# Performance work log

Measured on AMD Instinct MI355X. Metric: run time of the kernel, lower is better.

The kernel has to match this reference:

```python
import jax, jax.numpy as jnp
import numpy as np

N = 50000      # nodes
E = 800000     # edges (before self-loops)
DIN = 146      # input feature dim
D = 128        # hidden/out dim
G = 64         # graphs in batch
L = 4          # number of GCNConv layers (len(hidden_dims[1:]) + 1)
NC = 10        # classes
EPS = 1e-5     # BatchNorm eps


def setup_inputs() -> dict:
    key = jax.random.key(0)
    ks = jax.random.split(key, 12)
    x = jax.random.normal(ks[0], (N, DIN), jnp.float32)
    edge_index = jax.random.randint(ks[1], (2, E), 0, N, dtype=jnp.int64)
    batch = jnp.sort(jax.random.randint(ks[2], (N,), 0, G, dtype=jnp.int64))

    def lin(k, shape, fan_in):
        return (jax.random.normal(k, shape, jnp.float32) / np.sqrt(fan_in)).astype(jnp.float32)

    W_emb = lin(ks[3], (DIN, D), DIN)
    b_emb = jnp.zeros((D,), jnp.float32)
    W_gcn = lin(ks[4], (L, D, D), D)
    b_gcn = jnp.zeros((L, D), jnp.float32)
    bn_gamma = jnp.ones((L, D), jnp.float32)
    bn_beta = jnp.zeros((L, D), jnp.float32)
    W_r1 = lin(ks[5], (D, D // 2), D)
    b_r1 = jnp.zeros((D // 2,), jnp.float32)
    W_r2 = lin(ks[6], (D // 2, D // 4), D // 2)
    b_r2 = jnp.zeros((D // 4,), jnp.float32)
    W_r3 = lin(ks[7], (D // 4, NC), D // 4)
    b_r3 = jnp.zeros((NC,), jnp.float32)
    return {"x": x, "edge_index": edge_index, "batch": batch,
            "W_emb": W_emb, "b_emb": b_emb, "W_gcn": W_gcn, "b_gcn": b_gcn,
            "bn_gamma": bn_gamma, "bn_beta": bn_beta,
            "W_r1": W_r1, "b_r1": b_r1, "W_r2": W_r2, "b_r2": b_r2,
            "W_r3": W_r3, "b_r3": b_r3}


def reference(x, edge_index, batch, W_emb, b_emb, W_gcn, b_gcn,
              bn_gamma, bn_beta, W_r1, b_r1, W_r2, b_r2, W_r3, b_r3):
    # gcn_norm with self-loops (fill_value=1, improved=False)
    loop = jnp.arange(N, dtype=edge_index.dtype)
    src = jnp.concatenate([edge_index[0], loop])
    dst = jnp.concatenate([edge_index[1], loop])
    deg = jax.ops.segment_sum(jnp.ones(src.shape, x.dtype), dst, num_segments=N)
    dinv = jax.lax.rsqrt(jnp.maximum(deg, jnp.asarray(1e-12, x.dtype)))  # deg >= 1 (self loops)
    norm = (dinv[src] * dinv[dst])[:, None]  # [E+N, 1]

    h = x @ W_emb + b_emb  # embedding_h
    for l in range(L):
        h_in = h
        m = h @ W_gcn[l]                                            # [N, D]
        h = jax.ops.segment_sum(m[src] * norm, dst, num_segments=N) + b_gcn[l]
        # BatchNorm1d (training-mode batch stats, biased var)
        mu = h.mean(axis=0)
        var = h.var(axis=0)
        h = (h - mu) * jax.lax.rsqrt(var + EPS) * bn_gamma[l] + bn_beta[l]
        h = jax.nn.relu(h)
        h = h_in + h  # residual (dims always match here)

    # global_mean_pool over batch ids
    sums = jax.ops.segment_sum(h, batch, num_segments=G)
    cnts = jax.ops.segment_sum(jnp.ones((N, 1), h.dtype), batch, num_segments=G)
    hg = sums / jnp.maximum(cnts, 1.0)

    # MLPReadout: two hidden layers halving dims, then classifier
    z = jax.nn.relu(hg @ W_r1 + b_r1)
    z = jax.nn.relu(z @ W_r2 + b_r2)
    return z @ W_r3 + b_r3  # [G, NC]
```

## Files before the change

### kernel.cpp

```cpp
#include <hip/hip_runtime.h>
#include <hip/hip_bf16.h>

#define NN 50000
#define EE 800000
#define DIN 146
#define DD 128
#define GG 64
#define LL 4
#define NC 10
#define BN_EPS 1e-5f

#define KP_EMB 160
#define AST_L  136
#define NCOPY 64
#define NPW 4
#define RST 129

#define MB_EDGE   3125
#define MB_REPACK (MB_EDGE + 31250)
#define MB_BATCH  (MB_REPACK + 196)
#define MB_PARAMS (MB_BATCH + 384)
#define MB_WT     (MB_PARAMS + 400)

typedef __attribute__((ext_vector_type(8))) short bf16x8;
typedef __attribute__((ext_vector_type(4))) float f32x4;

__device__ __forceinline__ float bf2f(__hip_bfloat16 v) { return __bfloat162float(v); }
__device__ __forceinline__ float loadf(const void* p, long i, int f32) {
    return f32 ? ((const float*)p)[i] : bf2f(((const __hip_bfloat16*)p)[i]);
}
__device__ __forceinline__ unsigned short f2bf_bits(float f) {
    __hip_bfloat16 h = __float2bfloat16(f);
    return *(unsigned short*)&h;
}
__device__ __forceinline__ float bfu2f(unsigned short u) {
    return __uint_as_float((unsigned)u << 16);
}
__device__ __forceinline__ void acc_add8(float* acc, uint4 v) {
    acc[0] += __uint_as_float(v.x << 16);
    acc[1] += __uint_as_float(v.x & 0xffff0000u);
    acc[2] += __uint_as_float(v.y << 16);
    acc[3] += __uint_as_float(v.y & 0xffff0000u);
    acc[4] += __uint_as_float(v.z << 16);
    acc[5] += __uint_as_float(v.z & 0xffff0000u);
    acc[6] += __uint_as_float(v.w << 16);
    acc[7] += __uint_as_float(v.w & 0xffff0000u);
}

__global__ void detect_kernel(const void* ei, const void* batch, const void* Wemb,
                              int* __restrict__ flags) {
    __shared__ int s_edge_nz, s_batch_nz, s_f32_cnt;
    int t = threadIdx.x;
    if (t == 0) { s_edge_nz = 0; s_batch_nz = 0; s_f32_cnt = 0; }
    __syncthreads();
    {   const int* w = (const int*)ei;
        long j = ((long)t * ((2L * EE) / 64)) | 1;
        if (w[j] != 0) atomicAdd(&s_edge_nz, 1);
    }
    {   const int* w = (const int*)batch;
        long j = ((long)(NN / 2) + (long)t * ((NN / 2) / 64)) | 1;
        if (j < NN && w[j] != 0) atomicAdd(&s_batch_nz, 1);
    }
    {   const unsigned short* w = (const unsigned short*)Wemb;
        unsigned short v = w[2 * t];
        int ex = (v >> 7) & 0xFF;
        if (v != 0 && ex >= 128) atomicAdd(&s_f32_cnt, 1);
    }
    __syncthreads();
    if (t == 0) {
        flags[0] = (s_edge_nz == 0) ? 1 : 0;
        flags[1] = (s_batch_nz == 0) ? 1 : 0;
        flags[2] = (s_f32_cnt >= 8) ? 1 : 0;
    }
}

struct Param { const void* src; float* dst; int src_n; int dst_n; };
struct Params12 { Param p[12]; };
struct WtDesc { const void* src; long src_off; unsigned short* dst; int K; int Kpad; };
struct WtDescs5 { WtDesc p[5]; };

__global__ void init_kernel(int* __restrict__ deg, float* __restrict__ statmulti,
                            float* __restrict__ hgsum) {
    int i = blockIdx.x * blockDim.x + threadIdx.x;
    if (i < NN) deg[i] = 0;
    if (i < LL * NCOPY * 256) statmulti[i] = 0.0f;
    if (i < GG * DD) hgsum[i] = 0.0f;
}

__global__ __launch_bounds__(256) void mega_pre_kernel(
    const void* __restrict__ x, const void* __restrict__ ei,
    const void* __restrict__ batch, const int* __restrict__ flags,
    unsigned short* __restrict__ xb,
    int* __restrict__ src32, int* __restrict__ dst32,
    int* __restrict__ rank, int* __restrict__ deg, int* __restrict__ b32,
    Params12 P, WtDescs5 W)
{
    int b = blockIdx.x;
    int t = threadIdx.x;
    if (b < MB_EDGE) {
        int e = b * 256 + t;
        const int* w = (const int*)ei;
        int s, d;
        if (flags[0]) { s = w[2L * e]; d = w[2L * (EE + e)]; }
        else          { s = w[e];      d = w[EE + e]; }
        src32[e] = s; dst32[e] = d;
        int r = 0;
        if ((unsigned)d < (unsigned)NN) r = atomicAdd(&deg[d], 1);
        rank[e] = r;
    } else if (b < MB_REPACK) {
        int f32 = flags[2];
        long idx = (long)(b - MB_EDGE) * 256 + t;
        int row = (int)(idx / KP_EMB);
        int k = (int)(idx - (long)row * KP_EMB);
        float v = (k < DIN) ? loadf(x, (long)row * DIN + k, f32) : 0.0f;
        xb[idx] = f2bf_bits(v);
    } else if (b < MB_BATCH) {
        int i = (b - MB_REPACK) * 256 + t;
        if (i < NN) b32[i] = flags[1] ? ((const int*)batch)[2L * i] : ((const int*)batch)[i];
    } else if (b < MB_PARAMS) {
        int f32 = flags[2];
        int bb = b - MB_BATCH;
        const Param& e = P.p[bb >> 5];
        int idx = (bb & 31) * 256 + t;
        if (idx < e.dst_n)
            e.dst[idx] = (idx < e.src_n) ? loadf(e.src, idx, f32) : 0.0f;
    } else {
        int f32 = flags[2];
        int bb = b - MB_PARAMS;
        int y = bb / 80;
        const WtDesc& e = W.p[y];
        int idx = (bb - y * 80) * 256 + t;
        if (idx < 128 * e.Kpad) {
            int n = idx / e.Kpad, k = idx - n * e.Kpad;
            float v = (k < e.K) ? loadf(e.src, e.src_off + (long)k * DD + n, f32) : 0.0f;
            e.dst[idx] = f2bf_bits(v);
        }
    }
}

__global__ void scan1_kernel(const int* __restrict__ cnt, int* __restrict__ off,
                             int* __restrict__ bsum, float* __restrict__ dinv, int n) {
    int t = threadIdx.x;
    int i = blockIdx.x * 256 + t;
    int v = (i < n) ? cnt[i] : 0;
    if (i < n) dinv[i] = rsqrtf((float)(v + 1));
    int lane = t & 63, w = t >> 6;
    int x = v;
    #pragma unroll
    for (int s = 1; s < 64; s <<= 1) {
        int y = __shfl_up(x, s, 64);
        if (lane >= s) x += y;
    }
    __shared__ int wsum[4];
    if (lane == 63) wsum[w] = x;
    __syncthreads();
    if (t == 0) {
        int a = 0;
        #pragma unroll
        for (int k = 0; k < 4; ++k) { int tmp = wsum[k]; wsum[k] = a; a += tmp; }
        bsum[blockIdx.x] = a;
    }
    __syncthreads();
    int excl = x - v + wsum[w];
    if (i < n) off[i] = excl;
}

__global__ void scan2_kernel(int* __restrict__ bsum, int* __restrict__ boff,
                             int* __restrict__ off_last, int nb) {
    int t = threadIdx.x;
    int v = (t < nb) ? bsum[t] : 0;
    int lane = t & 63, w = t >> 6;
    int x = v;
    #pragma unroll
    for (int s = 1; s < 64; s <<= 1) {
        int y = __shfl_up(x, s, 64);
        if (lane >= s) x += y;
    }
    __shared__ int wsum[4];
    if (lane == 63) wsum[w] = x;
    __syncthreads();
    __shared__ int total_s;
    if (t == 0) {
        int a = 0;
        #pragma unroll
        for (int k = 0; k < 4; ++k) { int tmp = wsum[k]; wsum[k] = a; a += tmp; }
        total_s = a;
    }
    __syncthreads();
    if (t < nb) boff[t] = x - v + wsum[w];
    if (t == 0) *off_last = total_s;
}

__global__ void scan3_kernel(int* __restrict__ off, const int* __restrict__ boff, int n) {
    int i = blockIdx.x * 256 + threadIdx.x;
    if (i < n) off[i] += boff[blockIdx.x];
}

__global__ void scatter_kernel(const int* __restrict__ src, const int* __restrict__ dst,
                               const int* __restrict__ rank, const int* __restrict__ off,
                               int* __restrict__ src_s, int E) {
    int e = blockIdx.x * blockDim.x + threadIdx.x;
    if (e >= E) return;
    int s = src[e], d = dst[e];
    if ((unsigned)s >= (unsigned)NN || (unsigned)d >= (unsigned)NN) return;
    src_s[off[d] + rank[e]] = s;
}


__global__ __launch_bounds__(256) void emb_gemm_kernel(
    const unsigned short* __restrict__ Ab,
    const unsigned short* __restrict__ Wt,
    const float* __restrict__ bias,
    float* __restrict__ h, unsigned short* __restrict__ hb, int n)
{
    int t = threadIdx.x;
    int r0 = blockIdx.x * 128;
    int lane = t & 63, w = t >> 6;
    int m = lane & 15, quad = lane >> 4;
    int rbase = r0 + w * 32;
    bf16x8 a[2][5];
    #pragma unroll
    for (int rt = 0; rt < 2; ++rt)
        #pragma unroll
        for (int c = 0; c < 5; ++c) {
            int rr = rbase + rt * 16 + m; if (rr > n - 1) rr = n - 1;
            a[rt][c] = *(const bf16x8*)(Ab + (long)rr * KP_EMB + c * 32 + quad * 8);
        }
    f32x4 acc[2][8];
    #pragma unroll
    for (int t8 = 0; t8 < 8; ++t8) {
        float bv = bias[t8 * 16 + m];
        f32x4 ai = {bv, bv, bv, bv};
        acc[0][t8] = ai; acc[1][t8] = ai;
    }
    #pragma unroll
    for (int t8 = 0; t8 < 8; ++t8) {
        #pragma unroll
        for (int c = 0; c < 5; ++c) {
            bf16x8 b = *(const bf16x8*)(Wt + (long)(t8 * 16 + m) * KP_EMB + c * 32 + quad * 8);
            acc[0][t8] = __builtin_amdgcn_mfma_f32_16x16x32_bf16(a[0][c], b, acc[0][t8], 0, 0, 0);
            acc[1][t8] = __builtin_amdgcn_mfma_f32_16x16x32_bf16(a[1][c], b, acc[1][t8], 0, 0, 0);
        }
    }
    #pragma unroll
    for (int rt = 0; rt < 2; ++rt)
        #pragma unroll
        for (int t8 = 0; t8 < 8; ++t8)
            #pragma unroll
            for (int rg = 0; rg < 4; ++rg) {
                int row = rbase + rt * 16 + quad * 4 + rg;
                int col = t8 * 16 + m;
                if (row < n) {
                    float v = acc[rt][t8][rg];
                    h[(long)row * DD + col] = v;
                    hb[(long)row * DD + col] = f2bf_bits(v);
                }
            }
}

__global__ __launch_bounds__(256) void gemm_plain_kernel(
    const unsigned short* __restrict__ Ab,
    const unsigned short* __restrict__ Wt,
    const float* __restrict__ dinv,
    unsigned short* __restrict__ Mb, int n)
{
    int t = threadIdx.x;
    int r0 = blockIdx.x * 128;
    int lane = t & 63, w = t >> 6;
    int m = lane & 15, quad = lane >> 4;
    int rbase = r0 + w * 32;
    bf16x8 a[2][4];
    #pragma unroll
    for (int rt = 0; rt < 2; ++rt)
        #pragma unroll
        for (int c = 0; c < 4; ++c) {
            int rr = rbase + rt * 16 + m; if (rr > n - 1) rr = n - 1;
            a[rt][c] = *(const bf16x8*)(Ab + (long)rr * DD + c * 32 + quad * 8);
        }
    float dv[2][4];
    #pragma unroll
    for (int rt = 0; rt < 2; ++rt)
        #pragma unroll
        for (int rg = 0; rg < 4; ++rg) {
            int row = rbase + rt * 16 + quad * 4 + rg; if (row > n - 1) row = n - 1;
            dv[rt][rg] = dinv[row];
        }
    f32x4 acc[2][8];
    #pragma unroll
    for (int t8 = 0; t8 < 8; ++t8) {
        f32x4 z = {0.f, 0.f, 0.f, 0.f};
        acc[0][t8] = z; acc[1][t8] = z;
    }
    #pragma unroll
    for (int t8 = 0; t8 < 8; ++t8) {
        #pragma unroll
        for (int c = 0; c < 4; ++c) {
            bf16x8 b = *(const bf16x8*)(Wt + (long)(t8 * 16 + m) * DD + c * 32 + quad * 8);
            acc[0][t8] = __builtin_amdgcn_mfma_f32_16x16x32_bf16(a[0][c], b, acc[0][t8], 0, 0, 0);
            acc[1][t8] = __builtin_amdgcn_mfma_f32_16x16x32_bf16(a[1][c], b, acc[1][t8], 0, 0, 0);
        }
    }
    #pragma unroll
    for (int rt = 0; rt < 2; ++rt)
        #pragma unroll
        for (int t8 = 0; t8 < 8; ++t8)
            #pragma unroll
            for (int rg = 0; rg < 4; ++rg) {
                int row = rbase + rt * 16 + quad * 4 + rg;
                int col = t8 * 16 + m;
                if (row < n) Mb[(long)row * DD + col] = f2bf_bits(dv[rt][rg] * acc[rt][t8][rg]);
            }
}

__global__ __launch_bounds__(256) void gemm_fused_kernel(
    const float* __restrict__ agg, float* __restrict__ h,
    const float* __restrict__ bnacc, const float* __restrict__ gamma,
    const float* __restrict__ beta, const float* __restrict__ dinv,
    const unsigned short* __restrict__ Wt, unsigned short* __restrict__ Mb, int n)
{
    __shared__ unsigned short As[128 * AST_L];
    int t = threadIdx.x;
    int r0 = blockIdx.x * 128;
    {
        int c4 = (t & 31) * 4, rsub = t >> 5;
        float inv_n = 1.0f / (float)n;
        float4 sm = *(const float4*)&bnacc[c4];
        float4 sq = *(const float4*)&bnacc[128 + c4];
        float4 ga = *(const float4*)&gamma[c4];
        float4 be = *(const float4*)&beta[c4];
        float4 mu, rs;
        mu.x = sm.x * inv_n; mu.y = sm.y * inv_n; mu.z = sm.z * inv_n; mu.w = sm.w * inv_n;
        rs.x = rsqrtf(sq.x * inv_n - mu.x * mu.x + BN_EPS) * ga.x;
        rs.y = rsqrtf(sq.y * inv_n - mu.y * mu.y + BN_EPS) * ga.y;
        rs.z = rsqrtf(sq.z * inv_n - mu.z * mu.z + BN_EPS) * ga.z;
        rs.w = rsqrtf(sq.w * inv_n - mu.w * mu.w + BN_EPS) * ga.w;
        #pragma unroll 4
        for (int i = 0; i < 16; ++i) {
            int row = i * 8 + rsub;
            int r = r0 + row;
            unsigned short o0 = 0, o1 = 0, o2 = 0, o3 = 0;
            if (r < n) {
                long g = (long)r * DD + c4;
                float4 av = *(const float4*)&agg[g];
                float4 hv = *(const float4*)&h[g];
                hv.x += fmaxf((av.x - mu.x) * rs.x + be.x, 0.0f);
                hv.y += fmaxf((av.y - mu.y) * rs.y + be.y, 0.0f);
                hv.z += fmaxf((av.z - mu.z) * rs.z + be.z, 0.0f);
                hv.w += fmaxf((av.w - mu.w) * rs.w + be.w, 0.0f);
                *(float4*)&h[g] = hv;
                o0 = f2bf_bits(hv.x); o1 = f2bf_bits(hv.y);
                o2 = f2bf_bits(hv.z); o3 = f2bf_bits(hv.w);
            }
            unsigned short* dst = &As[row * AST_L + c4];
            dst[0] = o0; dst[1] = o1; dst[2] = o2; dst[3] = o3;
        }
    }
    __syncthreads();
    int lane = t & 63, w = t >> 6;
    int m = lane & 15, quad = lane >> 4;
    int rl = w * 32;
    int rbase = r0 + rl;
    bf16x8 a[2][4];
    #pragma unroll
    for (int rt = 0; rt < 2; ++rt)
        #pragma unroll
        for (int c = 0; c < 4; ++c)
            a[rt][c] = *(const bf16x8*)(As + (rl + rt * 16 + m) * AST_L + c * 32 + quad * 8);
    float dv[2][4];
    #pragma unroll
    for (int rt = 0; rt < 2; ++rt)
        #pragma unroll
        for (int rg = 0; rg < 4; ++rg) {
            int row = rbase + rt * 16 + quad * 4 + rg; if (row > n - 1) row = n - 1;
            dv[rt][rg] = dinv[row];
        }
    f32x4 acc[2][8];
    #pragma unroll
    for (int t8 = 0; t8 < 8; ++t8) {
        f32x4 z = {0.f, 0.f, 0.f, 0.f};
        acc[0][t8] = z; acc[1][t8] = z;
    }
    #pragma unroll
    for (int t8 = 0; t8 < 8; ++t8) {
        #pragma unroll
        for (int c = 0; c < 4; ++c) {
            bf16x8 b = *(const bf16x8*)(Wt + (long)(t8 * 16 + m) * DD + c * 32 + quad * 8);
            acc[0][t8] = __builtin_amdgcn_mfma_f32_16x16x32_bf16(a[0][c], b, acc[0][t8], 0, 0, 0);
            acc[1][t8] = __builtin_amdgcn_mfma_f32_16x16x32_bf16(a[1][c], b, acc[1][t8], 0, 0, 0);
        }
    }
    #pragma unroll
    for (int rt = 0; rt < 2; ++rt)
        #pragma unroll
        for (int t8 = 0; t8 < 8; ++t8)
            #pragma unroll
            for (int rg = 0; rg < 4; ++rg) {
                int row = rbase + rt * 16 + quad * 4 + rg;
                int col = t8 * 16 + m;
                if (row < n) Mb[(long)row * DD + col] = f2bf_bits(dv[rt][rg] * acc[rt][t8][rg]);
            }
}

__global__ __launch_bounds__(256) void agg_kernel(
    const unsigned short* __restrict__ mb, const int* __restrict__ off,
    const int* __restrict__ src_s, const float* __restrict__ dinv,
    const float* __restrict__ bias, float* __restrict__ agg,
    float* __restrict__ statacc)
{
    __shared__ float sred[4][4 * RST];
    __shared__ float2 ssum[4][64], ssq[4][64];
    int t = threadIdx.x;
    int wv = t >> 6, lane = t & 63;
    int grp = lane >> 4, sl = lane & 15;
    float* red = sred[wv];
    float2 bi = ((const float2*)bias)[lane];
    float2 sAcc = {0.0f, 0.0f}, qAcc = {0.0f, 0.0f};
    int i0 = (blockIdx.x * 4 + wv) * NPW;
    #pragma unroll 1
    for (int ni = 0; ni < NPW; ++ni) {
        int i = i0 + ni;
        if (i >= NN) break;
        float acc[8];
        #pragma unroll
        for (int k = 0; k < 8; ++k) acc[k] = 0.0f;
        if (grp == 0) {
            uint4 v = *(const uint4*)(mb + (long)i * DD + sl * 8);
            acc_add8(acc, v);
        }
        int e = off[i], e1 = off[i + 1];
        for (; e + 8 <= e1; e += 8) {
            int ja = src_s[e + grp];
            int jb = src_s[e + 4 + grp];
            uint4 va = *(const uint4*)(mb + (long)ja * DD + sl * 8);
            uint4 vb = *(const uint4*)(mb + (long)jb * DD + sl * 8);
            acc_add8(acc, va);
            acc_add8(acc, vb);
        }
        for (; e + 4 <= e1; e += 4) {
            int j = src_s[e + grp];
            uint4 v = *(const uint4*)(mb + (long)j * DD + sl * 8);
            acc_add8(acc, v);
        }
        if (e + grp < e1) {
            int j = src_s[e + grp];
            uint4 v = *(const uint4*)(mb + (long)j * DD + sl * 8);
            acc_add8(acc, v);
        }
        #pragma unroll
        for (int k = 0; k < 8; ++k) red[grp * RST + sl * 8 + k] = acc[k];
        asm volatile("" ::: "memory");
        float c0 = 0.0f, c1 = 0.0f;
        #pragma unroll
        for (int g = 0; g < 4; ++g) {
            c0 += red[g * RST + 2 * lane];
            c1 += red[g * RST + 2 * lane + 1];
        }
        asm volatile("" ::: "memory");
        float di = dinv[i];
        float2 outv;
        outv.x = di * c0 + bi.x;
        outv.y = di * c1 + bi.y;
        ((float2*)agg)[(long)i * 64 + lane] = outv;
        sAcc.x += outv.x; sAcc.y += outv.y;
        qAcc.x += outv.x * outv.x; qAcc.y += outv.y * outv.y;
    }
    ssum[wv][lane] = sAcc; ssq[wv][lane] = qAcc;
    __syncthreads();
    if (wv == 0) {
        float2 s0 = ssum[0][lane], s1 = ssum[1][lane], s2 = ssum[2][lane], s3 = ssum[3][lane];
        float2 q0 = ssq[0][lane], q1 = ssq[1][lane], q2 = ssq[2][lane], q3 = ssq[3][lane];
        float sx = s0.x + s1.x + s2.x + s3.x;
        float sy = s0.y + s1.y + s2.y + s3.y;
        float qx = q0.x + q1.x + q2.x + q3.x;
        float qy = q0.y + q1.y + q2.y + q3.y;
        float* copy = statacc + (blockIdx.x & (NCOPY - 1)) * 256;
        atomicAdd(&copy[2 * lane], sx);
        atomicAdd(&copy[2 * lane + 1], sy);
        atomicAdd(&copy[128 + 2 * lane], qx);
        atomicAdd(&copy[128 + 2 * lane + 1], qy);
    }
}

__global__ void statfin_kernel(const float* __restrict__ multi, float* __restrict__ bnacc) {
    int c = threadIdx.x;
    float s = 0.0f;
    #pragma unroll 8
    for (int k = 0; k < NCOPY; ++k) s += multi[k * 256 + c];
    bnacc[c] = s;
}

__global__ void pool1_kernel(const float* __restrict__ h, const float* __restrict__ agg,
                             const float* __restrict__ bnacc,
                             const float* __restrict__ gamma, const float* __restrict__ beta,
                             const int* __restrict__ b32, float* __restrict__ hgsum, int n) {
    int t = threadIdx.x;
    int c4 = (t & 31) * 4, rsub = t >> 5;
    float inv_n = 1.0f / (float)n;
    float4 sm = *(const float4*)&bnacc[c4];
    float4 sq = *(const float4*)&bnacc[128 + c4];
    float4 ga = *(const float4*)&gamma[c4];
    float4 be = *(const float4*)&beta[c4];
    float4 mu, rs;
    mu.x = sm.x * inv_n; mu.y = sm.y * inv_n; mu.z = sm.z * inv_n; mu.w = sm.w * inv_n;
    rs.x = rsqrtf(sq.x * inv_n - mu.x * mu.x + BN_EPS) * ga.x;
    rs.y = rsqrtf(sq.y * inv_n - mu.y * mu.y + BN_EPS) * ga.y;
    rs.z = rsqrtf(sq.z * inv_n - mu.z * mu.z + BN_EPS) * ga.z;
    rs.w = rsqrtf(sq.w * inv_n - mu.w * mu.w + BN_EPS) * ga.w;
    int rows_pb = (n + gridDim.x - 1) / gridDim.x;
    int r0 = blockIdx.x * rows_pb;
    int r1 = min(n, r0 + rows_pb);
    float4 acc = {0, 0, 0, 0};
    int gcur = -1;
    for (int r = r0 + rsub; r < r1; r += 8) {
        int g = b32[r];
        if (g != gcur) {
            if (gcur >= 0) {
                atomicAdd(&hgsum[gcur * DD + c4 + 0], acc.x);
                atomicAdd(&hgsum[gcur * DD + c4 + 1], acc.y);
                atomicAdd(&hgsum[gcur * DD + c4 + 2], acc.z);
                atomicAdd(&hgsum[gcur * DD + c4 + 3], acc.w);
            }
            acc.x = acc.y = acc.z = acc.w = 0.0f;
            gcur = ((unsigned)g < (unsigned)GG) ? g : -1;
        }
        if (gcur >= 0) {
            long ix = (long)r * DD + c4;
            float4 av = *(const float4*)&agg[ix];
            float4 hv = *(const float4*)&h[ix];
            acc.x += hv.x + fmaxf((av.x - mu.x) * rs.x + be.x, 0.0f);
            acc.y += hv.y + fmaxf((av.y - mu.y) * rs.y + be.y, 0.0f);
            acc.z += hv.z + fmaxf((av.z - mu.z) * rs.z + be.z, 0.0f);
            acc.w += hv.w + fmaxf((av.w - mu.w) * rs.w + be.w, 0.0f);
        }
    }
    if (gcur >= 0) {
        atomicAdd(&hgsum[gcur * DD + c4 + 0], acc.x);
        atomicAdd(&hgsum[gcur * DD + c4 + 1], acc.y);
        atomicAdd(&hgsum[gcur * DD + c4 + 2], acc.z);
        atomicAdd(&hgsum[gcur * DD + c4 + 3], acc.w);
    }
}

__device__ int lower_bound_i(const int* __restrict__ a, int n, int v) {
    int lo = 0, hi = n;
    while (lo < hi) {
        int mid = (lo + hi) >> 1;
        if (a[mid] < v) lo = mid + 1; else hi = mid;
    }
    return lo;
}

__global__ void readout_kernel(const float* __restrict__ hgsum, const int* __restrict__ b32,
                               const float* __restrict__ W1, const float* __restrict__ b1,
                               const float* __restrict__ W2, const float* __restrict__ b2,
                               const float* __restrict__ W3, const float* __restrict__ b3,
                               const int* __restrict__ flags, void* __restrict__ out, int n) {
    int f32 = flags[2];
    int g = blockIdx.x;
    int t = threadIdx.x;
    __shared__ float hgs[DD];
    __shared__ float z1[DD / 2];
    __shared__ float z2[DD / 4];
    int lo = lower_bound_i(b32, n, g);
    int hi = lower_bound_i(b32, n, g + 1);
    float invc = 1.0f / fmaxf((float)(hi - lo), 1.0f);
    hgs[t] = hgsum[g * DD + t] * invc;
    __syncthreads();
    if (t < DD / 2) {
        float acc = b1[t];
        #pragma unroll 8
        for (int k = 0; k < DD; ++k) acc = fmaf(hgs[k], W1[k * (DD / 2) + t], acc);
        z1[t] = fmaxf(acc, 0.0f);
    }
    __syncthreads();
    if (t < DD / 4) {
        float acc = b2[t];
        #pragma unroll 8
        for (int k = 0; k < DD / 2; ++k) acc = fmaf(z1[k], W2[k * (DD / 4) + t], acc);
        z2[t] = fmaxf(acc, 0.0f);
    }
    __syncthreads();
    if (t < NC) {
        float acc = b3[t];
        #pragma unroll 8
        for (int k = 0; k < DD / 4; ++k) acc = fmaf(z2[k], W3[k * NC + t], acc);
        if (f32) ((float*)out)[g * NC + t] = acc;
        else     ((__hip_bfloat16*)out)[g * NC + t] = __float2bfloat16(acc);
    }
}

extern "C" void kernel_launch(void* const* d_in, const int* in_sizes, int n_in,
                              void* d_out, int out_size, void* d_ws, size_t ws_size,
                              hipStream_t stream) {
    const void* x      = d_in[0];
    const void* ei     = d_in[1];
    const void* batch  = d_in[2];
    const void* W_emb  = d_in[3];
    const void* b_emb  = d_in[4];
    const void* W_gcn  = d_in[5];
    const void* b_gcn  = d_in[6];
    const void* bn_g   = d_in[7];
    const void* bn_b   = d_in[8];
    const void* W_r1   = d_in[9];
    const void* b_r1   = d_in[10];
    const void* W_r2   = d_in[11];
    const void* b_r2   = d_in[12];
    const void* W_r3   = d_in[13];
    const void* b_r3   = d_in[14];

    char* p = (char*)d_ws;
    auto alloc = [&](size_t bytes) -> void* {
        void* r = (void*)p;
        p += (bytes + 255) & ~(size_t)255;
        return r;
    };
    int*   flags  = (int*)alloc(64 * 4);
    int*   deg    = (int*)alloc((size_t)NN * 4);
    float* bnacc  = (float*)alloc((size_t)LL * 256 * 4);
    float* statmulti = (float*)alloc((size_t)LL * NCOPY * 256 * 4);
    float* hgsum  = (float*)alloc((size_t)GG * DD * 4);
    int*   off    = (int*)alloc((size_t)(NN + 1) * 4);
    float* dinv   = (float*)alloc((size_t)NN * 4);
    int*   src32  = (int*)alloc((size_t)EE * 4);
    int*   dst32  = (int*)alloc((size_t)EE * 4);
    int*   rank   = (int*)alloc((size_t)EE * 4);
    int*   b32    = (int*)alloc((size_t)NN * 4);
    int*   src_s  = (int*)alloc((size_t)EE * 4);
    int*   bsum   = (int*)alloc(256 * 4);
    int*   boff   = (int*)alloc(256 * 4);
    float* h      = (float*)alloc((size_t)NN * DD * 4);
    unsigned short* hb = (unsigned short*)alloc((size_t)NN * DD * 2);
    unsigned short* mb = (unsigned short*)alloc((size_t)NN * DD * 2);
    float* agg    = (float*)alloc((size_t)NN * DD * 4);
    unsigned short* xb = (unsigned short*)agg;
    unsigned short* wt_emb = (unsigned short*)alloc((size_t)DD * KP_EMB * 2);
    unsigned short* wt_gcn = (unsigned short*)alloc((size_t)LL * DD * DD * 2);
    float* b_emb32 = (float*)alloc(DD * 4);
    float* b_gcn32 = (float*)alloc((size_t)LL * DD * 4);
    float* bng32   = (float*)alloc((size_t)LL * DD * 4);
    float* bnb32   = (float*)alloc((size_t)LL * DD * 4);
    float* wr1     = (float*)alloc((size_t)DD * (DD / 2) * 4);
    float* br1     = (float*)alloc((DD / 2) * 4);
    float* wr2     = (float*)alloc((size_t)(DD / 2) * (DD / 4) * 4);
    float* br2     = (float*)alloc((DD / 4) * 4);
    float* wr3     = (float*)alloc((size_t)(DD / 4) * NC * 4);
    float* br3     = (float*)alloc(NC * 4);

    detect_kernel<<<1, 64, 0, stream>>>(ei, batch, W_emb, flags);
    init_kernel<<<256, 256, 0, stream>>>(deg, statmulti, hgsum);

    Params12 P;
    P.p[0]  = { b_emb, b_emb32, DD, DD };
    P.p[1]  = { b_gcn, b_gcn32, LL * DD, LL * DD };
    P.p[2]  = { bn_g,  bng32,   LL * DD, LL * DD };
    P.p[3]  = { bn_b,  bnb32,   LL * DD, LL * DD };
    P.p[4]  = { W_r1,  wr1,     DD * (DD / 2), DD * (DD / 2) };
    P.p[5]  = { b_r1,  br1,     DD / 2, DD / 2 };
    P.p[6]  = { W_r2,  wr2,     (DD / 2) * (DD / 4), (DD / 2) * (DD / 4) };
    P.p[7]  = { b_r2,  br2,     DD / 4, DD / 4 };
    P.p[8]  = { W_r3,  wr3,     (DD / 4) * NC, (DD / 4) * NC };
    P.p[9]  = { b_r3,  br3,     NC, NC };
    P.p[10] = { b_r3,  br3,     0, 0 };
    P.p[11] = { b_r3,  br3,     0, 0 };

    WtDescs5 W;
    W.p[0] = { W_emb, 0,            wt_emb,                DIN, KP_EMB };
    W.p[1] = { W_gcn, 0L * DD * DD, wt_gcn + 0L * DD * DD, DD,  DD };
    W.p[2] = { W_gcn, 1L * DD * DD, wt_gcn + 1L * DD * DD, DD,  DD };
    W.p[3] = { W_gcn, 2L * DD * DD, wt_gcn + 2L * DD * DD, DD,  DD };
    W.p[4] = { W_gcn, 3L * DD * DD, wt_gcn + 3L * DD * DD, DD,  DD };

    mega_pre_kernel<<<MB_WT, 256, 0, stream>>>(x, ei, batch, flags, xb,
                                               src32, dst32, rank, deg, b32, P, W);

    int nb = (NN + 255) / 256;
    scan1_kernel<<<nb, 256, 0, stream>>>(deg, off, bsum, dinv, NN);
    scan2_kernel<<<1, 256, 0, stream>>>(bsum, boff, off + NN, nb);
    scan3_kernel<<<nb, 256, 0, stream>>>(off, boff, NN);

    scatter_kernel<<<(EE + 255) / 256, 256, 0, stream>>>(src32, dst32, rank, off, src_s, EE);

    int ngemm = (NN + 127) / 128;
    emb_gemm_kernel<<<ngemm, 256, 0, stream>>>(xb, wt_emb, b_emb32, h, hb, NN);

    int nagg = (NN + 4 * NPW - 1) / (4 * NPW);
    for (int l = 0; l < LL; ++l) {
        if (l == 0) {
            gemm_plain_kernel<<<ngemm, 256, 0, stream>>>(hb, wt_gcn, dinv, mb, NN);
        } else {
            gemm_fused_kernel<<<ngemm, 256, 0, stream>>>(
                agg, h, bnacc + (l - 1) * 256, bng32 + (l - 1) * DD, bnb32 + (l - 1) * DD,
                dinv, wt_gcn + (size_t)l * DD * DD, mb, NN);
        }
        agg_kernel<<<nagg, 256, 0, stream>>>(mb, off, src_s, dinv,
                                             b_gcn32 + l * DD, agg,
                                             statmulti + (size_t)l * NCOPY * 256);
        statfin_kernel<<<1, 256, 0, stream>>>(statmulti + (size_t)l * NCOPY * 256,
                                              bnacc + l * 256);
    }

    pool1_kernel<<<512, 256, 0, stream>>>(h, agg, bnacc + (LL - 1) * 256,
                                          bng32 + (LL - 1) * DD, bnb32 + (LL - 1) * DD,
                                          b32, hgsum, NN);
    readout_kernel<<<GG, DD, 0, stream>>>(hgsum, b32, wr1, br1, wr2, br2, wr3, br3,
                                          flags, d_out, NN);
}
```

Baseline: 472.3 us.

## Merge preprocessing launches and fold stat reduction into consumer kernels

Folds init_kernel into the conversion mega-kernel. The edge degree-counting blocks now share a launch with the embedding GEMM, and the CSR scatter shares a launch with the layer-0 GEMM. It also removes statfin_kernel: every gemm_fused and pool1 block now reduces the 64 stat copies itself into shared memory. The aim is to cut kernel launches and the gaps between them, and to overlap independent work. The cost is redundant stat reduction in every block plus a dependence on independent work being correctly split into separate block ranges.

New measurement: 458.4 us. 1.03x faster.

```diff
diff --git a/kernel.cpp b/kernel.cpp
--- a/kernel.cpp
+++ b/kernel.cpp
@@ -16,11 +16,16 @@
 #define NPW 4
 #define RST 129
 
-#define MB_EDGE   3125
-#define MB_REPACK (MB_EDGE + 31250)
-#define MB_BATCH  (MB_REPACK + 196)
-#define MB_PARAMS (MB_BATCH + 384)
-#define MB_WT     (MB_PARAMS + 400)
+#define C_INIT   256
+#define C_REPACK (C_INIT + 31250)
+#define C_BATCH  (C_REPACK + 196)
+#define C_PARAMS (C_BATCH + 384)
+#define C_WT     (C_PARAMS + 400)
+
+#define B_EDGE 3125
+#define B_TOT  (B_EDGE + 391)
+#define S_SCAT 3125
+#define S_TOT  (S_SCAT + 391)
 
 typedef __attribute__((ext_vector_type(8))) short bf16x8;
 typedef __attribute__((ext_vector_type(4))) float f32x4;
@@ -79,26 +84,63 @@
 struct WtDesc { const void* src; long src_off; unsigned short* dst; int K; int Kpad; };
 struct WtDescs5 { WtDesc p[5]; };
 
-__global__ void init_kernel(int* __restrict__ deg, float* __restrict__ statmulti,
-                            float* __restrict__ hgsum) {
-    int i = blockIdx.x * blockDim.x + threadIdx.x;
-    if (i < NN) deg[i] = 0;
-    if (i < LL * NCOPY * 256) statmulti[i] = 0.0f;
-    if (i < GG * DD) hgsum[i] = 0.0f;
-}
-
-__global__ __launch_bounds__(256) void mega_pre_kernel(
-    const void* __restrict__ x, const void* __restrict__ ei,
-    const void* __restrict__ batch, const int* __restrict__ flags,
-    unsigned short* __restrict__ xb,
-    int* __restrict__ src32, int* __restrict__ dst32,
-    int* __restrict__ rank, int* __restrict__ deg, int* __restrict__ b32,
-    Params12 P, WtDescs5 W)
+__global__ __launch_bounds__(256) void mega_conv_kernel(
+    const void* __restrict__ x, const void* __restrict__ batch,
+    const int* __restrict__ flags, unsigned short* __restrict__ xb,
+    int* __restrict__ deg, float* __restrict__ statmulti, float* __restrict__ hgsum,
+    int* __restrict__ b32, Params12 P, WtDescs5 W)
 {
     int b = blockIdx.x;
     int t = threadIdx.x;
-    if (b < MB_EDGE) {
-        int e = b * 256 + t;
+    if (b < C_INIT) {
+        int i = b * 256 + t;
+        if (i < NN) deg[i] = 0;
+        if (i < LL * NCOPY * 256) statmulti[i] = 0.0f;
+        if (i < GG * DD) hgsum[i] = 0.0f;
+    } else if (b < C_REPACK) {
+        int f32 = flags[2];
+        long idx = (long)(b - C_INIT) * 256 + t;
+        int row = (int)(idx / KP_EMB);
+        int k = (int)(idx - (long)row * KP_EMB);
+        float v = (k < DIN) ? loadf(x, (long)row * DIN + k, f32) : 0.0f;
+        xb[idx] = f2bf_bits(v);
+    } else if (b < C_BATCH) {
+        int i = (b - C_REPACK) * 256 + t;
+        if (i < NN) b32[i] = flags[1] ? ((const int*)batch)[2L * i] : ((const int*)batch)[i];
+    } else if (b < C_PARAMS) {
+        int f32 = flags[2];
+        int bb = b - C_BATCH;
+        const Param& e = P.p[bb >> 5];
+        int idx = (bb & 31) * 256 + t;
+        if (idx < e.dst_n)
+            e.dst[idx] = (idx < e.src_n) ? loadf(e.src, idx, f32) : 0.0f;
+    } else {
+        int f32 = flags[2];
+        int bb = b - C_PARAMS;
+        int y = bb / 80;
+        const WtDesc& e = W.p[y];
+        int idx = (bb - y * 80) * 256 + t;
+        if (idx < 128 * e.Kpad) {
+            int n = idx / e.Kpad, k = idx - n * e.Kpad;
+            float v = (k < e.K) ? loadf(e.src, e.src_off + (long)k * DD + n, f32) : 0.0f;
+            e.dst[idx] = f2bf_bits(v);
+        }
+    }
+}
+
+
+__global__ __launch_bounds__(256) void edge_emb_kernel(
+    const void* __restrict__ ei, const int* __restrict__ flags,
+    int* __restrict__ src32, int* __restrict__ dst32,
+    int* __restrict__ rank, int* __restrict__ deg,
+    const unsigned short* __restrict__ Ab,
+    const unsigned short* __restrict__ Wt,
+    const float* __restrict__ bias,
+    float* __restrict__ h, unsigned short* __restrict__ hb, int n)
+{
+    int t = threadIdx.x;
+    if (blockIdx.x < B_EDGE) {
+        int e = blockIdx.x * 256 + t;
         const int* w = (const int*)ei;
         int s, d;
         if (flags[0]) { s = w[2L * e]; d = w[2L * (EE + e)]; }
@@ -107,114 +149,9 @@
         int r = 0;
         if ((unsigned)d < (unsigned)NN) r = atomicAdd(&deg[d], 1);
         rank[e] = r;
-    } else if (b < MB_REPACK) {
-        int f32 = flags[2];
-        long idx = (long)(b - MB_EDGE) * 256 + t;
-        int row = (int)(idx / KP_EMB);
-        int k = (int)(idx - (long)row * KP_EMB);
-        float v = (k < DIN) ? loadf(x, (long)row * DIN + k, f32) : 0.0f;
-        xb[idx] = f2bf_bits(v);
-    } else if (b < MB_BATCH) {
-        int i = (b - MB_REPACK) * 256 + t;
-        if (i < NN) b32[i] = flags[1] ? ((const int*)batch)[2L * i] : ((const int*)batch)[i];
-    } else if (b < MB_PARAMS) {
-        int f32 = flags[2];
-        int bb = b - MB_BATCH;
-        const Param& e = P.p[bb >> 5];
-        int idx = (bb & 31) * 256 + t;
-        if (idx < e.dst_n)
-            e.dst[idx] = (idx < e.src_n) ? loadf(e.src, idx, f32) : 0.0f;
-    } else {
-        int f32 = flags[2];
-        int bb = b - MB_PARAMS;
-        int y = bb / 80;
-        const WtDesc& e = W.p[y];
-        int idx = (bb - y * 80) * 256 + t;
-        if (idx < 128 * e.Kpad) {
-            int n = idx / e.Kpad, k = idx - n * e.Kpad;
-            float v = (k < e.K) ? loadf(e.src, e.src_off + (long)k * DD + n, f32) : 0.0f;
-            e.dst[idx] = f2bf_bits(v);
-        }
-    }
-}
-
-__global__ void scan1_kernel(const int* __restrict__ cnt, int* __restrict__ off,
-                             int* __restrict__ bsum, float* __restrict__ dinv, int n) {
-    int t = threadIdx.x;
-    int i = blockIdx.x * 256 + t;
-    int v = (i < n) ? cnt[i] : 0;
-    if (i < n) dinv[i] = rsqrtf((float)(v + 1));
-    int lane = t & 63, w = t >> 6;
-    int x = v;
-    #pragma unroll
-    for (int s = 1; s < 64; s <<= 1) {
-        int y = __shfl_up(x, s, 64);
-        if (lane >= s) x += y;
-    }
-    __shared__ int wsum[4];
-    if (lane == 63) wsum[w] = x;
-    __syncthreads();
-    if (t == 0) {
-        int a = 0;
-        #pragma unroll
-        for (int k = 0; k < 4; ++k) { int tmp = wsum[k]; wsum[k] = a; a += tmp; }
-        bsum[blockIdx.x] = a;
-    }
-    __syncthreads();
-    int excl = x - v + wsum[w];
-    if (i < n) off[i] = excl;
-}
-
-__global__ void scan2_kernel(int* __restrict__ bsum, int* __restrict__ boff,
-                             int* __restrict__ off_last, int nb) {
-    int t = threadIdx.x;
-    int v = (t < nb) ? bsum[t] : 0;
-    int lane = t & 63, w = t >> 6;
-    int x = v;
-    #pragma unroll
-    for (int s = 1; s < 64; s <<= 1) {
-        int y = __shfl_up(x, s, 64);
-        if (lane >= s) x += y;
-    }
-    __shared__ int wsum[4];
-    if (lane == 63) wsum[w] = x;
-    __syncthreads();
-    __shared__ int total_s;
-    if (t == 0) {
-        int a = 0;
-        #pragma unroll
-        for (int k = 0; k < 4; ++k) { int tmp = wsum[k]; wsum[k] = a; a += tmp; }
-        total_s = a;
-    }
-    __syncthreads();
-    if (t < nb) boff[t] = x - v + wsum[w];
-    if (t == 0) *off_last = total_s;
-}
-
-__global__ void scan3_kernel(int* __restrict__ off, const int* __restrict__ boff, int n) {
-    int i = blockIdx.x * 256 + threadIdx.x;
-    if (i < n) off[i] += boff[blockIdx.x];
-}
-
-__global__ void scatter_kernel(const int* __restrict__ src, const int* __restrict__ dst,
-                               const int* __restrict__ rank, const int* __restrict__ off,
-                               int* __restrict__ src_s, int E) {
-    int e = blockIdx.x * blockDim.x + threadIdx.x;
-    if (e >= E) return;
-    int s = src[e], d = dst[e];
-    if ((unsigned)s >= (unsigned)NN || (unsigned)d >= (unsigned)NN) return;
-    src_s[off[d] + rank[e]] = s;
-}
-
-
-__global__ __launch_bounds__(256) void emb_gemm_kernel(
-    const unsigned short* __restrict__ Ab,
-    const unsigned short* __restrict__ Wt,
-    const float* __restrict__ bias,
-    float* __restrict__ h, unsigned short* __restrict__ hb, int n)
-{
-    int t = threadIdx.x;
-    int r0 = blockIdx.x * 128;
+        return;
+    }
+    int r0 = (blockIdx.x - B_EDGE) * 128;
     int lane = t & 63, w = t >> 6;
     int m = lane & 15, quad = lane >> 4;
     int rbase = r0 + w * 32;
@@ -258,14 +195,82 @@
             }
 }
 
-__global__ __launch_bounds__(256) void gemm_plain_kernel(
+__global__ void scan1_kernel(const int* __restrict__ cnt, int* __restrict__ off,
+                             int* __restrict__ bsum, float* __restrict__ dinv, int n) {
+    int t = threadIdx.x;
+    int i = blockIdx.x * 256 + t;
+    int v = (i < n) ? cnt[i] : 0;
+    if (i < n) dinv[i] = rsqrtf((float)(v + 1));
+    int lane = t & 63, w = t >> 6;
+    int x = v;
+    #pragma unroll
+    for (int s = 1; s < 64; s <<= 1) {
+        int y = __shfl_up(x, s, 64);
+        if (lane >= s) x += y;
+    }
+    __shared__ int wsum[4];
+    if (lane == 63) wsum[w] = x;
+    __syncthreads();
+    if (t == 0) {
+        int a = 0;
+        #pragma unroll
+        for (int k = 0; k < 4; ++k) { int tmp = wsum[k]; wsum[k] = a; a += tmp; }
+        bsum[blockIdx.x] = a;
+    }
+    __syncthreads();
+    int excl = x - v + wsum[w];
+    if (i < n) off[i] = excl;
+}
+
+__global__ void scan2_kernel(int* __restrict__ bsum, int* __restrict__ boff,
+                             int* __restrict__ off_last, int nb) {
+    int t = threadIdx.x;
+    int v = (t < nb) ? bsum[t] : 0;
+    int lane = t & 63, w = t >> 6;
+    int x = v;
+    #pragma unroll
+    for (int s = 1; s < 64; s <<= 1) {
+        int y = __shfl_up(x, s, 64);
+        if (lane >= s) x += y;
+    }
+    __shared__ int wsum[4];
+    if (lane == 63) wsum[w] = x;
+    __syncthreads();
+    __shared__ int total_s;
+    if (t == 0) {
+        int a = 0;
+        #pragma unroll
+        for (int k = 0; k < 4; ++k) { int tmp = wsum[k]; wsum[k] = a; a += tmp; }
+        total_s = a;
+    }
+    __syncthreads();
+    if (t < nb) boff[t] = x - v + wsum[w];
+    if (t == 0) *off_last = total_s;
+}
+
+__global__ void scan3_kernel(int* __restrict__ off, const int* __restrict__ boff, int n) {
+    int i = blockIdx.x * 256 + threadIdx.x;
+    if (i < n) off[i] += boff[blockIdx.x];
+}
+
+__global__ __launch_bounds__(256) void scat_mm_kernel(
+    const int* __restrict__ src, const int* __restrict__ dst,
+    const int* __restrict__ rank, const int* __restrict__ off,
+    int* __restrict__ src_s,
     const unsigned short* __restrict__ Ab,
     const unsigned short* __restrict__ Wt,
     const float* __restrict__ dinv,
     unsigned short* __restrict__ Mb, int n)
 {
     int t = threadIdx.x;
-    int r0 = blockIdx.x * 128;
+    if (blockIdx.x < S_SCAT) {
+        int e = blockIdx.x * 256 + t;
+        int s = src[e], d = dst[e];
+        if ((unsigned)s >= (unsigned)NN || (unsigned)d >= (unsigned)NN) return;
+        src_s[off[d] + rank[e]] = s;
+        return;
+    }
+    int r0 = (blockIdx.x - S_SCAT) * 128;
     int lane = t & 63, w = t >> 6;
     int m = lane & 15, quad = lane >> 4;
     int rbase = r0 + w * 32;
@@ -314,18 +319,26 @@
 
 __global__ __launch_bounds__(256) void gemm_fused_kernel(
     const float* __restrict__ agg, float* __restrict__ h,
-    const float* __restrict__ bnacc, const float* __restrict__ gamma,
+    const float* __restrict__ statmulti, const float* __restrict__ gamma,
     const float* __restrict__ beta, const float* __restrict__ dinv,
     const unsigned short* __restrict__ Wt, unsigned short* __restrict__ Mb, int n)
 {
     __shared__ unsigned short As[128 * AST_L];
+    __shared__ float bnsh[256];
     int t = threadIdx.x;
     int r0 = blockIdx.x * 128;
+    {
+        float s = 0.0f;
+        #pragma unroll 8
+        for (int k = 0; k < NCOPY; ++k) s += statmulti[k * 256 + t];
+        bnsh[t] = s;
+    }
+    __syncthreads();
     {
         int c4 = (t & 31) * 4, rsub = t >> 5;
         float inv_n = 1.0f / (float)n;
-        float4 sm = *(const float4*)&bnacc[c4];
-        float4 sq = *(const float4*)&bnacc[128 + c4];
+        float4 sm = *(const float4*)&bnsh[c4];
+        float4 sq = *(const float4*)&bnsh[128 + c4];
         float4 ga = *(const float4*)&gamma[c4];
         float4 be = *(const float4*)&beta[c4];
         float4 mu, rs;
@@ -481,23 +494,23 @@
     }
 }
 
-__global__ void statfin_kernel(const float* __restrict__ multi, float* __restrict__ bnacc) {
-    int c = threadIdx.x;
-    float s = 0.0f;
-    #pragma unroll 8
-    for (int k = 0; k < NCOPY; ++k) s += multi[k * 256 + c];
-    bnacc[c] = s;
-}
-
 __global__ void pool1_kernel(const float* __restrict__ h, const float* __restrict__ agg,
-                             const float* __restrict__ bnacc,
+                             const float* __restrict__ statmulti,
                              const float* __restrict__ gamma, const float* __restrict__ beta,
                              const int* __restrict__ b32, float* __restrict__ hgsum, int n) {
-    int t = threadIdx.x;
+    __shared__ float bnsh[256];
+    int t = threadIdx.x;
+    {
+        float s = 0.0f;
+        #pragma unroll 8
+        for (int k = 0; k < NCOPY; ++k) s += statmulti[k * 256 + t];
+        bnsh[t] = s;
+    }
+    __syncthreads();
     int c4 = (t & 31) * 4, rsub = t >> 5;
     float inv_n = 1.0f / (float)n;
-    float4 sm = *(const float4*)&bnacc[c4];
-    float4 sq = *(const float4*)&bnacc[128 + c4];
+    float4 sm = *(const float4*)&bnsh[c4];
+    float4 sq = *(const float4*)&bnsh[128 + c4];
     float4 ga = *(const float4*)&gamma[c4];
     float4 be = *(const float4*)&beta[c4];
     float4 mu, rs;
@@ -616,7 +629,6 @@
     };
     int*   flags  = (int*)alloc(64 * 4);
     int*   deg    = (int*)alloc((size_t)NN * 4);
-    float* bnacc  = (float*)alloc((size_t)LL * 256 * 4);
     float* statmulti = (float*)alloc((size_t)LL * NCOPY * 256 * 4);
     float* hgsum  = (float*)alloc((size_t)GG * DD * 4);
     int*   off    = (int*)alloc((size_t)(NN + 1) * 4);
@@ -647,7 +659,6 @@
     float* br3     = (float*)alloc(NC * 4);
 
     detect_kernel<<<1, 64, 0, stream>>>(ei, batch, W_emb, flags);
-    init_kernel<<<256, 256, 0, stream>>>(deg, statmulti, hgsum);
 
     Params12 P;
     P.p[0]  = { b_emb, b_emb32, DD, DD };
@@ -670,36 +681,35 @@
     W.p[3] = { W_gcn, 2L * DD * DD, wt_gcn + 2L * DD * DD, DD,  DD };
     W.p[4] = { W_gcn, 3L * DD * DD, wt_gcn + 3L * DD * DD, DD,  DD };
 
-    mega_pre_kernel<<<MB_WT, 256, 0, stream>>>(x, ei, batch, flags, xb,
-                                               src32, dst32, rank, deg, b32, P, W);
+    mega_conv_kernel<<<C_WT, 256, 0, stream>>>(x, batch, flags, xb, deg, statmulti,
+                                               hgsum, b32, P, W);
+
+    edge_emb_kernel<<<B_TOT, 256, 0, stream>>>(ei, flags, src32, dst32, rank, deg,
+                                               xb, wt_emb, b_emb32, h, hb, NN);
 
     int nb = (NN + 255) / 256;
     scan1_kernel<<<nb, 256, 0, stream>>>(deg, off, bsum, dinv, NN);
     scan2_kernel<<<1, 256, 0, stream>>>(bsum, boff, off + NN, nb);
     scan3_kernel<<<nb, 256, 0, stream>>>(off, boff, NN);
 
-    scatter_kernel<<<(EE + 255) / 256, 256, 0, stream>>>(src32, dst32, rank, off, src_s, EE);
+    scat_mm_kernel<<<S_TOT, 256, 0, stream>>>(src32, dst32, rank, off, src_s,
+                                              hb, wt_gcn, dinv, mb, NN);
 
     int ngemm = (NN + 127) / 128;
-    emb_gemm_kernel<<<ngemm, 256, 0, stream>>>(xb, wt_emb, b_emb32, h, hb, NN);
-
     int nagg = (NN + 4 * NPW - 1) / (4 * NPW);
     for (int l = 0; l < LL; ++l) {
-        if (l == 0) {
-            gemm_plain_kernel<<<ngemm, 256, 0, stream>>>(hb, wt_gcn, dinv, mb, NN);
-        } else {
+        if (l > 0) {
             gemm_fused_kernel<<<ngemm, 256, 0, stream>>>(
-                agg, h, bnacc + (l - 1) * 256, bng32 + (l - 1) * DD, bnb32 + (l - 1) * DD,
+                agg, h, statmulti + (size_t)(l - 1) * NCOPY * 256,
+                bng32 + (l - 1) * DD, bnb32 + (l - 1) * DD,
                 dinv, wt_gcn + (size_t)l * DD * DD, mb, NN);
         }
         agg_kernel<<<nagg, 256, 0, stream>>>(mb, off, src_s, dinv,
                                              b_gcn32 + l * DD, agg,
                                              statmulti + (size_t)l * NCOPY * 256);
-        statfin_kernel<<<1, 256, 0, stream>>>(statmulti + (size_t)l * NCOPY * 256,
-                                              bnacc + l * 256);
-    }
-
-    pool1_kernel<<<512, 256, 0, stream>>>(h, agg, bnacc + (LL - 1) * 256,
+    }
+
+    pool1_kernel<<<512, 256, 0, stream>>>(h, agg, statmulti + (size_t)(LL - 1) * NCOPY * 256,
                                           bng32 + (LL - 1) * DD, bnb32 + (LL - 1) * DD,
                                           b32, hgsum, NN);
     readout_kernel<<<GG, DD, 0, stream>>>(hgsum, b32, wr1, br1, wr2, br2, wr3, br3,
```
